# Kernel tuning notes

Hardware: AMD Instinct MI355X
Metric: run time of the kernel (lower is better)

Reference implementation:

```python
import jax, jax.numpy as jnp
import numpy as np

N_STEPS = 128        # params['n_steps']
NOISE_SCALE = 0.01   # params['noise_scale']
DIMS_X = 16
HID = 512
BATCH = 32768
DIMS_IN = 2 * DIMS_X + 1  # cond_x1=True: cat([t, x_t, x_1])


def _linear_init(key, fan_in, fan_out):
    # torch nn.Linear default: U(-1/sqrt(fan_in), 1/sqrt(fan_in))
    bound = 1.0 / np.sqrt(fan_in)
    kw, kb = jax.random.split(key)
    w = jax.random.uniform(kw, (fan_in, fan_out), jnp.float32, -bound, bound)
    b = jax.random.uniform(kb, (fan_out,), jnp.float32, -bound, bound)
    return w, b


def setup_inputs() -> dict:
    key = jax.random.key(0)
    ks = jax.random.split(key, 6)
    w0, b0 = _linear_init(ks[0], DIMS_IN, HID)
    w1, b1 = _linear_init(ks[1], HID, HID)
    w2, b2 = _linear_init(ks[2], HID, HID)
    w3, b3 = _linear_init(ks[3], HID, HID)
    w4, b4 = _linear_init(ks[4], HID, DIMS_X)
    x_1 = jax.random.normal(ks[5], (BATCH, DIMS_X), jnp.float32)
    return {"x_1": x_1, "w0": w0, "b0": b0, "w1": w1, "b1": b1,
            "w2": w2, "b2": b2, "w3": w3, "b3": b3, "w4": w4, "b4": b4}


def reference(x_1, w0, b0, w1, b1, w2, b2, w3, b3, w4, b4):
    dtype = x_1.dtype
    steps = jnp.linspace(1.0, 0.0, N_STEPS).astype(dtype)
    t_arr = steps[:-1]       # t
    tprev_arr = steps[1:]    # tprev (< t)
    noise_key = jax.random.key(42)
    ones_col = jnp.ones((x_1.shape[0], 1), dtype)

    def net(t, x_t):
        h = jnp.concatenate([t * ones_col, x_t, x_1], axis=-1)  # [B, 2*Dx+1]
        for w, b in ((w0, b0), (w1, b1), (w2, b2), (w3, b3)):
            h = jax.nn.relu(h @ w + b)
        return h @ w4 + b4  # [B, Dx]

    def body(x_t, inp):
        t, tprev, i = inp
        drift = net(t, x_t)
        pred_x0 = x_t - t * drift
        x_new = (t - tprev) / t * pred_x0 + tprev / t * x_t
        noise = jax.random.normal(jax.random.fold_in(noise_key, i), x_t.shape, dtype)
        x_new = x_new + jnp.sqrt(NOISE_SCALE * tprev * (t - tprev) / t) * noise
        return x_new, None

    x0 = jax.lax.stop_gradient(x_1)  # x_t = x_1.detach()
    x_final, _ = jax.lax.scan(body, x0, (t_arr, tprev_arr, jnp.arange(N_STEPS - 1)))
    return x_final
```

## Files before the change

### kernel.cpp

```cpp
#include <hip/hip_runtime.h>

typedef _Float16 f16;
typedef __attribute__((ext_vector_type(4))) _Float16 f16x4;
typedef __attribute__((ext_vector_type(8))) _Float16 f16x8;
typedef __attribute__((ext_vector_type(4))) float f32x4;

#define HID 512
#define DIMS_X 16
#define NSTEPS 127
#define BM 128
#define BATCH 32768
#define LDST 520

#define OFF_W0 0
#define OFF_W1 32768
#define OFF_W2 (32768 + 262144)
#define OFF_W3 (32768 + 2 * 262144)
#define OFF_W4 (32768 + 3 * 262144)

__global__ void pack_w_kernel(const float* __restrict__ w, f16* __restrict__ out,
                              int K, int Kpad, int N) {
    int idx = blockIdx.x * blockDim.x + threadIdx.x;
    if (idx >= Kpad * N) return;
    int k = idx / N, n = idx - k * N;
    float v = (k < K) ? w[k * N + n] : 0.0f;
    out[(((k >> 3) * N) + n) * 8 + (k & 7)] = (f16)v;
}

__global__ void pack_w0_kernel(const float* __restrict__ w, f16* __restrict__ out) {
    int idx = blockIdx.x * blockDim.x + threadIdx.x;
    if (idx >= 64 * HID) return;
    int kn = idx / HID, n = idx - kn * HID;
    float v;
    if (kn < 32) v = w[(kn + 1) * HID + n];
    else if (kn == 32) v = w[n];
    else v = 0.0f;
    out[(((kn >> 3) * HID) + n) * 8 + (kn & 7)] = (f16)v;
}

__device__ __forceinline__ unsigned rotl32(unsigned x, int r) {
    return (x << r) | (x >> (32 - r));
}

__device__ __forceinline__ void threefry2x32(unsigned k0, unsigned k1,
                                             unsigned c0, unsigned c1,
                                             unsigned& o0, unsigned& o1) {
    unsigned ks2 = k0 ^ k1 ^ 0x1BD11BDAu;
    unsigned x0 = c0 + k0, x1 = c1 + k1;
#define TF_R(rot) { x0 += x1; x1 = rotl32(x1, rot); x1 ^= x0; }
    TF_R(13) TF_R(15) TF_R(26) TF_R(6)
    x0 += k1;  x1 += ks2 + 1u;
    TF_R(17) TF_R(29) TF_R(16) TF_R(24)
    x0 += ks2; x1 += k0 + 2u;
    TF_R(13) TF_R(15) TF_R(26) TF_R(6)
    x0 += k0;  x1 += k1 + 3u;
    TF_R(17) TF_R(29) TF_R(16) TF_R(24)
    x0 += k1;  x1 += ks2 + 4u;
    TF_R(13) TF_R(15) TF_R(26) TF_R(6)
    x0 += ks2; x1 += k0 + 5u;
#undef TF_R
    o0 = x0; o1 = x1;
}

__device__ __forceinline__ float erfinv_xla(float x) {
    float w = -log1pf(-x * x);
    float p;
    if (w < 5.0f) {
        w = w - 2.5f;
        p = 2.81022636e-08f;
        p = fmaf(p, w, 3.43273939e-07f);
        p = fmaf(p, w, -3.5233877e-06f);
        p = fmaf(p, w, -4.39150654e-06f);
        p = fmaf(p, w, 0.00021858087f);
        p = fmaf(p, w, -0.00125372503f);
        p = fmaf(p, w, -0.00417768164f);
        p = fmaf(p, w, 0.246640727f);
        p = fmaf(p, w, 1.50140941f);
    } else {
        w = sqrtf(w) - 3.0f;
        p = -0.000200214257f;
        p = fmaf(p, w, 0.000100950558f);
        p = fmaf(p, w, 0.00134934322f);
        p = fmaf(p, w, -0.00367342844f);
        p = fmaf(p, w, 0.00573950773f);
        p = fmaf(p, w, -0.0076224613f);
        p = fmaf(p, w, 0.00943887047f);
        p = fmaf(p, w, 1.00167406f);
        p = fmaf(p, w, 2.83297682f);
    }
    return p * x;
}

__device__ __forceinline__ unsigned lds_off(int row, int colByte) {
    return (unsigned)(row * (LDST * 2) + colByte);
}

#define KC_BODY(kc, wc, wn, NKC)                                                      \
    {                                                                                 \
        if ((kc) + 1 < (NKC)) {                                                       \
            const f16* wk = wbase + (size_t)((kc) + 1) * (4 * HID * 8);               \
            wn[0] = *(const f16x8*)(wk);                                              \
            wn[1] = *(const f16x8*)(wk + 128);                                        \
            wn[2] = *(const f16x8*)(wk + 256);                                        \
            wn[3] = *(const f16x8*)(wk + 384);                                        \
        }                                                                             \
        f16x8 afr[8];                                                                 \
        _Pragma("unroll")                                                             \
        for (int tb = 0; tb < 8; ++tb)                                                \
            afr[tb] = *(const f16x8*)((const char*)act +                              \
                                      lds_off(tb * 16 + lc, (kc) * 64 + lk * 16));    \
        _Pragma("unroll")                                                             \
        for (int tn = 0; tn < 4; ++tn)                                                \
            _Pragma("unroll")                                                         \
            for (int tb = 0; tb < 8; ++tb)                                            \
                acc[tn][tb] = __builtin_amdgcn_mfma_f32_16x16x32_f16(                 \
                    wc[tn], afr[tb], acc[tn][tb], 0, 0, 0);                           \
    }

template <int NKC>
__device__ __forceinline__ void layer_swapped(f16* act, const f16* __restrict__ Wp,
                                              const float* bias_l,
                                              int wv, int lk, int lc) {
    f32x4 acc[4][8];
#pragma unroll
    for (int tn = 0; tn < 4; ++tn) {
        f32x4 bv = *(const f32x4*)(bias_l + wv * 64 + tn * 16 + lk * 4);
#pragma unroll
        for (int tb = 0; tb < 8; ++tb) acc[tn][tb] = bv;
    }

    const f16* wbase = Wp + ((size_t)lk * HID + wv * 64 + lc) * 8;
    f16x8 wA[4], wB[4];
    wA[0] = *(const f16x8*)(wbase);
    wA[1] = *(const f16x8*)(wbase + 128);
    wA[2] = *(const f16x8*)(wbase + 256);
    wA[3] = *(const f16x8*)(wbase + 384);

#pragma unroll 1
    for (int kp = 0; kp < NKC / 2; ++kp) {
        KC_BODY(2 * kp, wA, wB, NKC)
        KC_BODY(2 * kp + 1, wB, wA, NKC)
    }

    __syncthreads();
#pragma unroll
    for (int tn = 0; tn < 4; ++tn)
#pragma unroll
        for (int tb = 0; tb < 8; ++tb) {
            f16x4 v;
#pragma unroll
            for (int r = 0; r < 4; ++r) v[r] = (f16)fmaxf(acc[tn][tb][r], 0.0f);
            int brow = tb * 16 + lc;
            int nb = (wv * 64 + tn * 16 + lk * 4) * 2;
            *(f16x4*)((char*)act + lds_off(brow, nb)) = v;
        }
    __syncthreads();
}

__global__ __launch_bounds__(512, 2) void didi_main(
    const float* __restrict__ x1g,
    const float* __restrict__ b0g, const float* __restrict__ b1g,
    const float* __restrict__ b2g, const float* __restrict__ b3g,
    const float* __restrict__ b4g,
    const f16* __restrict__ wsp,
    float* __restrict__ outg) {
    __shared__ __align__(16) f16 act[BM * LDST];
    __shared__ __align__(16) float bias_lds[4 * HID];

    const f16* W0p = wsp + OFF_W0;
    const f16* W1p = wsp + OFF_W1;
    const f16* W2p = wsp + OFF_W2;
    const f16* W3p = wsp + OFF_W3;
    const f16* W4p = wsp + OFF_W4;

    const int tid = threadIdx.x;
    const int wv = tid >> 6;
    const int ln = tid & 63;
    const int lk = ln >> 4;
    const int lc = ln & 15;
    const int rowBase = blockIdx.x * BM;

    for (int o = tid; o < HID; o += 512) {
        bias_lds[o] = b0g[o];
        bias_lds[HID + o] = b1g[o];
        bias_lds[2 * HID + o] = b2g[o];
        bias_lds[3 * HID + o] = b3g[o];
    }
    f32x4 bias4v = *(const f32x4*)(b4g + lk * 4);

    {
        f16x8 z = {};
        for (int o = tid; o < (BM * LDST) / 8; o += 512)
            *(f16x8*)(act + o * 8) = z;
    }
    __syncthreads();

    f32x4 xr, x1r;
    {
        int grow = rowBase + wv * 16 + lc;
        x1r = *(const f32x4*)(x1g + grow * DIMS_X + lk * 4);
        xr = x1r;
        int lrow = wv * 16 + lc;
        f16x4 xf, x1f;
#pragma unroll
        for (int r = 0; r < 4; ++r) { xf[r] = (f16)xr[r]; x1f[r] = (f16)x1r[r]; }
        *(f16x4*)((char*)act + lds_off(lrow, lk * 8)) = xf;
        *(f16x4*)((char*)act + lds_off(lrow, 32 + lk * 8)) = x1f;
        if (lk == 0)
            *(f16*)((char*)act + lds_off(lrow, 64)) = (f16)1.0f;
    }
    __syncthreads();

    const float dstep = -1.0f / 127.0f;

#pragma unroll 1
    for (int i = 0; i < NSTEPS; ++i) {
        layer_swapped<2>(act, W0p, bias_lds, wv, lk, lc);
        layer_swapped<16>(act, W1p, bias_lds + HID, wv, lk, lc);
        layer_swapped<16>(act, W2p, bias_lds + 2 * HID, wv, lk, lc);
        layer_swapped<16>(act, W3p, bias_lds + 3 * HID, wv, lk, lc);

        float t  = 1.0f + (float)i * dstep;
        float tp = (i == NSTEPS - 1) ? 0.0f : 1.0f + (float)(i + 1) * dstep;

        {
            f32x4 acc4 = bias4v;
#pragma unroll 4
            for (int kc = 0; kc < 16; ++kc) {
                f16x8 w4fr = *(const f16x8*)(W4p + ((size_t)(kc * 4 + lk) * 16 + lc) * 8);
                f16x8 afr = *(const f16x8*)((const char*)act + lds_off(wv * 16 + lc, kc * 64 + lk * 16));
                acc4 = __builtin_amdgcn_mfma_f32_16x16x32_f16(w4fr, afr, acc4, 0, 0, 0);
            }
            float ca = (t - tp) / t;
            float cb = tp / t;
            float sig = sqrtf(((0.01f * tp) * (t - tp)) / t);
            unsigned fk0, fk1;
            threefry2x32(0u, 42u, 0u, (unsigned)i, fk0, fk1);
            int grow = rowBase + wv * 16 + lc;
            int lrow = wv * 16 + lc;
            f16x4 xf, x1f;
#pragma unroll
            for (int r = 0; r < 4; ++r) {
                float drift = acc4[r];
                unsigned flat = (unsigned)grow * 16u + (unsigned)(lk * 4 + r);
                unsigned o0, o1;
                threefry2x32(fk0, fk1, 0u, flat, o0, o1);
                unsigned bits = o0 ^ o1;
                float u01 = __uint_as_float((bits >> 9) | 0x3f800000u) - 1.0f;
                float u = u01 * 2.0f + (-0.99999994f);
                u = fmaxf(-0.99999994f, u);
                float nz = 1.4142135623730951f * erfinv_xla(u);
                float x = xr[r];
                float pred = x - t * drift;
                float xn = ca * pred + cb * x;
                xn = xn + sig * nz;
                xr[r] = xn;
                xf[r] = (f16)xn;
                x1f[r] = (f16)x1r[r];
            }
            *(f16x4*)((char*)act + lds_off(lrow, lk * 8)) = xf;
            *(f16x4*)((char*)act + lds_off(lrow, 32 + lk * 8)) = x1f;
            if (lk == 0)
                *(f16*)((char*)act + lds_off(lrow, 64)) = (f16)tp;
        }
        __syncthreads();
    }

    {
        int grow = rowBase + wv * 16 + lc;
        *(f32x4*)(outg + grow * DIMS_X + lk * 4) = xr;
    }
}

extern "C" void kernel_launch(void* const* d_in, const int* in_sizes, int n_in,
                              void* d_out, int out_size, void* d_ws, size_t ws_size,
                              hipStream_t stream) {
    const float* x1 = (const float*)d_in[0];
    const float* w0 = (const float*)d_in[1];
    const float* b0 = (const float*)d_in[2];
    const float* w1 = (const float*)d_in[3];
    const float* b1 = (const float*)d_in[4];
    const float* w2 = (const float*)d_in[5];
    const float* b2 = (const float*)d_in[6];
    const float* w3 = (const float*)d_in[7];
    const float* b3 = (const float*)d_in[8];
    const float* w4 = (const float*)d_in[9];
    const float* b4 = (const float*)d_in[10];
    f16* ws = (f16*)d_ws;

    hipLaunchKernelGGL(pack_w0_kernel, dim3(128), dim3(256), 0, stream, w0, ws + OFF_W0);
    hipLaunchKernelGGL(pack_w_kernel, dim3(1024), dim3(256), 0, stream, w1, ws + OFF_W1, 512, 512, 512);
    hipLaunchKernelGGL(pack_w_kernel, dim3(1024), dim3(256), 0, stream, w2, ws + OFF_W2, 512, 512, 512);
    hipLaunchKernelGGL(pack_w_kernel, dim3(1024), dim3(256), 0, stream, w3, ws + OFF_W3, 512, 512, 512);
    hipLaunchKernelGGL(pack_w_kernel, dim3(32), dim3(256), 0, stream, w4, ws + OFF_W4, 512, 512, 16);

    hipLaunchKernelGGL(didi_main, dim3(BATCH / BM), dim3(512), 0, stream,
                       x1, b0, b1, b2, b3, b4, (const f16*)ws, (float*)d_out);
}
```

Baseline: 5.705 ms.

## Split each layer's batch tile into two row halves to shrink accumulators

Each hidden layer now runs as two passes over 64-row halves of the 128-row activation tile. Each pass uses a 4x4 accumulator array instead of 4x8, halving accumulator register use, and writes its ReLU output back in place after a barrier. An extra barrier is added before the output layer. In exchange, every layer's weight fragments are streamed from global memory twice per block, and a half now waits at a barrier before its in-place write.

```diff
diff --git a/kernel.cpp b/kernel.cpp
--- a/kernel.cpp
+++ b/kernel.cpp
@@ -104,57 +104,73 @@
             wn[2] = *(const f16x8*)(wk + 256);                                        \
             wn[3] = *(const f16x8*)(wk + 384);                                        \
         }                                                                             \
-        f16x8 afr[8];                                                                 \
+        f16x8 afr[4];                                                                 \
         _Pragma("unroll")                                                             \
-        for (int tb = 0; tb < 8; ++tb)                                                \
+        for (int tb = 0; tb < 4; ++tb)                                                \
             afr[tb] = *(const f16x8*)((const char*)act +                              \
-                                      lds_off(tb * 16 + lc, (kc) * 64 + lk * 16));    \
+                lds_off(rowOff + tb * 16 + lc, (kc) * 64 + lk * 16));                 \
         _Pragma("unroll")                                                             \
         for (int tn = 0; tn < 4; ++tn)                                                \
             _Pragma("unroll")                                                         \
-            for (int tb = 0; tb < 8; ++tb)                                            \
+            for (int tb = 0; tb < 4; ++tb)                                            \
                 acc[tn][tb] = __builtin_amdgcn_mfma_f32_16x16x32_f16(                 \
                     wc[tn], afr[tb], acc[tn][tb], 0, 0, 0);                           \
     }
 
-template <int NKC>
-__device__ __forceinline__ void layer_swapped(f16* act, const f16* __restrict__ Wp,
-                                              const float* bias_l,
-                                              int wv, int lk, int lc) {
-    f32x4 acc[4][8];
+__device__ __forceinline__ void init_acc4(f32x4 (&acc)[4][4], const float* bias_l,
+                                          int wv, int lk) {
 #pragma unroll
     for (int tn = 0; tn < 4; ++tn) {
         f32x4 bv = *(const f32x4*)(bias_l + wv * 64 + tn * 16 + lk * 4);
 #pragma unroll
-        for (int tb = 0; tb < 8; ++tb) acc[tn][tb] = bv;
-    }
-
+        for (int tb = 0; tb < 4; ++tb) acc[tn][tb] = bv;
+    }
+}
+
+template <int NKC>
+__device__ __forceinline__ void mfma_group(f32x4 (&acc)[4][4], const f16* act,
+                                           const f16* __restrict__ Wp, int rowOff,
+                                           int wv, int lk, int lc) {
     const f16* wbase = Wp + ((size_t)lk * HID + wv * 64 + lc) * 8;
     f16x8 wA[4], wB[4];
     wA[0] = *(const f16x8*)(wbase);
     wA[1] = *(const f16x8*)(wbase + 128);
     wA[2] = *(const f16x8*)(wbase + 256);
     wA[3] = *(const f16x8*)(wbase + 384);
-
 #pragma unroll 1
     for (int kp = 0; kp < NKC / 2; ++kp) {
         KC_BODY(2 * kp, wA, wB, NKC)
         KC_BODY(2 * kp + 1, wB, wA, NKC)
     }
-
+}
+
+__device__ __forceinline__ void epi_group(f32x4 (&acc)[4][4], f16* act, int rowOff,
+                                          int wv, int lk, int lc) {
+#pragma unroll
+    for (int tn = 0; tn < 4; ++tn)
+#pragma unroll
+        for (int tb = 0; tb < 4; ++tb) {
+            f16x4 v;
+#pragma unroll
+            for (int r = 0; r < 4; ++r) v[r] = (f16)fmaxf(acc[tn][tb][r], 0.0f);
+            *(f16x4*)((char*)act + lds_off(rowOff + tb * 16 + lc,
+                                           (wv * 64 + tn * 16 + lk * 4) * 2)) = v;
+        }
+}
+
+template <int NKC>
+__device__ __forceinline__ void layer_pipe(f16* act, const f16* __restrict__ Wp,
+                                           const float* bias_l,
+                                           int wv, int lk, int lc) {
+    f32x4 acc[4][4];
+    init_acc4(acc, bias_l, wv, lk);
+    mfma_group<NKC>(acc, act, Wp, 0, wv, lk, lc);
     __syncthreads();
-#pragma unroll
-    for (int tn = 0; tn < 4; ++tn)
-#pragma unroll
-        for (int tb = 0; tb < 8; ++tb) {
-            f16x4 v;
-#pragma unroll
-            for (int r = 0; r < 4; ++r) v[r] = (f16)fmaxf(acc[tn][tb][r], 0.0f);
-            int brow = tb * 16 + lc;
-            int nb = (wv * 64 + tn * 16 + lk * 4) * 2;
-            *(f16x4*)((char*)act + lds_off(brow, nb)) = v;
-        }
+    epi_group(acc, act, 0, wv, lk, lc);
+    init_acc4(acc, bias_l, wv, lk);
+    mfma_group<NKC>(acc, act, Wp, 64, wv, lk, lc);
     __syncthreads();
+    epi_group(acc, act, 64, wv, lk, lc);
 }
 
 __global__ __launch_bounds__(512, 2) void didi_main(
@@ -215,10 +231,11 @@
 
 #pragma unroll 1
     for (int i = 0; i < NSTEPS; ++i) {
-        layer_swapped<2>(act, W0p, bias_lds, wv, lk, lc);
-        layer_swapped<16>(act, W1p, bias_lds + HID, wv, lk, lc);
-        layer_swapped<16>(act, W2p, bias_lds + 2 * HID, wv, lk, lc);
-        layer_swapped<16>(act, W3p, bias_lds + 3 * HID, wv, lk, lc);
+        layer_pipe<2>(act, W0p, bias_lds, wv, lk, lc);
+        layer_pipe<16>(act, W1p, bias_lds + HID, wv, lk, lc);
+        layer_pipe<16>(act, W2p, bias_lds + 2 * HID, wv, lk, lc);
+        layer_pipe<16>(act, W3p, bias_lds + 3 * HID, wv, lk, lc);
+        __syncthreads();
 
         float t  = 1.0f + (float)i * dstep;
         float tp = (i == NSTEPS - 1) ? 0.0f : 1.0f + (float)(i + 1) * dstep;
```

Measured after the change: 5.910 ms. +3.6%, slower.
